# Optimization experiments

Hardware: AMD Instinct MI355X
Metric: run time of the kernel (lower is better)

## Reference

```python
import jax, jax.numpy as jnp
import numpy as np

E, H, NH, FFN, OUT = 4096, 512, 4, 1024, 1
HD = H // NH
LN_EPS = 1e-5


def setup_inputs() -> dict:
    key = jax.random.key(0)
    ks = jax.random.split(key, 20)
    s = 1.0 / np.sqrt(H)
    inp = {
        'x': jax.random.normal(ks[0], (E, H), jnp.float32),
        'edge_index': jax.random.randint(ks[1], (2, E), 0, E, jnp.int64),
        # DMPNN message linear
        'W_msg': jax.random.normal(ks[2], (H, H), jnp.float32) * s,
        'b_msg': jnp.zeros((H,), jnp.float32),
        # GRUCell weights (torch layout: [3H, H], gates r,z,n)
        'W_ih': jax.random.normal(ks[3], (3 * H, H), jnp.float32) * s,
        'b_ih': jnp.zeros((3 * H,), jnp.float32),
        'W_hh': jax.random.normal(ks[4], (3 * H, H), jnp.float32) * s,
        'b_hh': jnp.zeros((3 * H,), jnp.float32),
        # MultiheadAttention combined in-proj [3H, H] and out-proj [H, H]
        'W_in_proj': jax.random.normal(ks[5], (3 * H, H), jnp.float32) * s,
        'b_in_proj': jnp.zeros((3 * H,), jnp.float32),
        'W_out_proj': jax.random.normal(ks[6], (H, H), jnp.float32) * s,
        'b_out_proj': jnp.zeros((H,), jnp.float32),
        # LayerNorm
        'ln_g': jnp.ones((H,), jnp.float32),
        'ln_b': jnp.zeros((H,), jnp.float32),
        # GlobalAttention output linear
        'W_lin': jax.random.normal(ks[7], (H, H), jnp.float32) * s,
        'b_lin': jnp.zeros((H,), jnp.float32),
        # FFN: Linear(H->FFN), ReLU, Linear(FFN->OUT)
        'W_f1': jax.random.normal(ks[8], (FFN, H), jnp.float32) * s,
        'b_f1': jnp.zeros((FFN,), jnp.float32),
        'W_f2': jax.random.normal(ks[9], (OUT, FFN), jnp.float32) * (1.0 / np.sqrt(FFN)),
        'b_f2': jnp.zeros((OUT,), jnp.float32),
    }
    return inp


def reference(x, edge_index, W_msg, b_msg, W_ih, b_ih, W_hh, b_hh,
              W_in_proj, b_in_proj, W_out_proj, b_out_proj, ln_g, ln_b,
              W_lin, b_lin, W_f1, b_f1, W_f2, b_f2):
    # ---- DMPNNLayer: message + scatter-add aggregation + GRUCell update ----
    msg = jax.nn.relu(x @ W_msg.T + b_msg)                       # [E, H]
    agg = jnp.zeros_like(x).at[edge_index[1]].add(msg)           # scatter-add to dst edges
    gi = agg @ W_ih.T + b_ih                                     # [E, 3H]
    gh = x @ W_hh.T + b_hh                                       # [E, 3H]
    ir, iz, inn = jnp.split(gi, 3, axis=-1)
    hr, hz, hn = jnp.split(gh, 3, axis=-1)
    r = jax.nn.sigmoid(ir + hr)
    z = jax.nn.sigmoid(iz + hz)
    n = jnp.tanh(inn + r * hn)
    h = (1.0 - z) * n + z * x                                    # [E, H] updated edges
    # ---- GlobalAttention: MHA(h,h,h) + residual LN + relu(linear) ----
    qkv = h @ W_in_proj.T + b_in_proj                            # [E, 3H]
    q, k, v = jnp.split(qkv, 3, axis=-1)
    split_heads = lambda t: t.reshape(E, NH, HD).transpose(1, 0, 2)  # [NH, E, HD]
    q, k, v = split_heads(q), split_heads(k), split_heads(v)
    scale = np.float32(1.0 / np.sqrt(HD))
    attn = jax.nn.softmax(jnp.einsum('hqd,hkd->hqk', q, k) * scale, axis=-1)
    o = jnp.einsum('hqk,hkd->hqd', attn, v).transpose(1, 0, 2).reshape(E, H)
    o = o @ W_out_proj.T + b_out_proj
    y = o + h
    mu = jnp.mean(y, axis=-1, keepdims=True)
    var = jnp.mean((y - mu) ** 2, axis=-1, keepdims=True)
    yn = (y - mu) / jnp.sqrt(var + LN_EPS) * ln_g + ln_b
    g = jax.nn.relu(yn @ W_lin.T + b_lin)                        # [E, H]
    # ---- FFN ----
    f = jax.nn.relu(g @ W_f1.T + b_f1)                           # [E, FFN]
    return f @ W_f2.T + b_f2                                     # [E, OUT]
```

## Files before the change

### kernel.cpp

```cpp
#include <hip/hip_runtime.h>

typedef unsigned short ushort_t;
typedef __attribute__((ext_vector_type(8))) short short8;
typedef __attribute__((ext_vector_type(4))) float float4v;

#define E_N   4096
#define H_N   512
#define NH_N  4
#define HD_N  128
#define FFN_N 1024
#define H3_N  1536

__device__ __forceinline__ float bf2f(ushort_t u) {
  union { unsigned u; float f; } v; v.u = ((unsigned)u) << 16; return v.f;
}
__device__ __forceinline__ ushort_t f2bf(float f) {
  union { float f; unsigned u; } v; v.f = f;
  unsigned r = v.u + 0x7fffu + ((v.u >> 16) & 1u);
  return (ushort_t)(r >> 16);
}
__device__ __forceinline__ float fexp2(float x) {
  return __builtin_amdgcn_exp2f(x);
}
__device__ __forceinline__ uint4 cvt8(const float* p) {
  float4 a = *(const float4*)p;
  float4 b = *(const float4*)(p + 4);
  union { ushort_t u[8]; uint4 v; } pk;
  pk.u[0] = f2bf(a.x); pk.u[1] = f2bf(a.y); pk.u[2] = f2bf(a.z); pk.u[3] = f2bf(a.w);
  pk.u[4] = f2bf(b.x); pk.u[5] = f2bf(b.y); pk.u[6] = f2bf(b.z); pk.u[7] = f2bf(b.w);
  return pk.v;
}

__device__ __forceinline__ void gload16(const void* g, void* l) {
  __builtin_amdgcn_global_load_lds(
      (const __attribute__((address_space(1))) unsigned*)g,
      (__attribute__((address_space(3))) unsigned*)l, 16, 0, 0);
}

__global__ __launch_bounds__(256) void prep_kernel(
    const float* __restrict__ x,
    const float* __restrict__ wmsg, const float* __restrict__ wih,
    const float* __restrict__ whh,  const float* __restrict__ win,
    const float* __restrict__ wout, const float* __restrict__ wlin,
    const float* __restrict__ wf1,  ushort_t* __restrict__ dst,
    float4* __restrict__ agg)
{
  int b = blockIdx.x;
  if (b < 2048) {
    agg[(size_t)b * 256 + threadIdx.x] = make_float4(0.f, 0.f, 0.f, 0.f);
    return;
  }
  size_t o = ((size_t)(b - 2048) * 256 + threadIdx.x) * 8;
  const float* s;
  if      (o < 2097152) s = x    + o;
  else if (o < 2359296) s = wmsg + (o - 2097152);
  else if (o < 3145728) s = wih  + (o - 2359296);
  else if (o < 3932160) s = whh  + (o - 3145728);
  else if (o < 4718592) s = win  + (o - 3932160);
  else if (o < 4980736) s = wout + (o - 4718592);
  else if (o < 5242880) s = wlin + (o - 4980736);
  else                  s = wf1  + (o - 5242880);
  *(uint4*)(dst + o) = cvt8(s);
}

__global__ __launch_bounds__(256) void cvt_agg_kernel(
    const float* __restrict__ agg, ushort_t* __restrict__ aggb) {
  size_t o = ((size_t)blockIdx.x * 256 + threadIdx.x) * 8;
  *(uint4*)(aggb + o) = cvt8(agg + o);
}

__global__ __launch_bounds__(256) void f2red_kernel(
    const float* __restrict__ pf, const float* __restrict__ b2,
    float* __restrict__ out) {
  int i = blockIdx.x * 256 + threadIdx.x;
  float s = b2[0];
#pragma unroll
  for (int k = 0; k < 32; k++) s += pf[(size_t)i * 32 + k];
  out[i] = s;
}

enum { MODE_MSG = 0, MODE_GI = 1, MODE_GH = 2, MODE_QKV = 3, MODE_OUT = 4,
       MODE_LIN = 5, MODE_F1 = 6 };

template <int MODE, int BM>
__global__ __launch_bounds__(256, (BM == 64 ? 4 : 3)) void gemm_bt(
    const ushort_t* __restrict__ A, const ushort_t* __restrict__ W,
    const float* __restrict__ bias, int K,
    float* __restrict__ outf, ushort_t* __restrict__ outb,
    const int* __restrict__ edge, float* __restrict__ aggf,
    const ushort_t* __restrict__ hres,
    ushort_t* __restrict__ qb, ushort_t* __restrict__ kb,
    ushort_t* __restrict__ vt, const float* __restrict__ wf2)
{
  constexpr int MI   = BM / 32;
  constexpr int ASZ  = BM * 128;
  constexpr int BSZ  = 64 * 128;
  constexpr int NCHA = BM / 8;
  constexpr int NCH  = NCHA + 8;

  __shared__ ushort_t As[2][BM * 64];
  __shared__ ushort_t Bs[2][64 * 64];

  const int tid  = threadIdx.x;
  const int lane = tid & 63;
  const int wave = tid >> 6;
  const int quad = lane >> 4;
  const int l15  = lane & 15;
  const int m0 = blockIdx.x * BM;
  const int n0 = blockIdx.y * 64;
  const int wm = (wave >> 1) * (BM / 2);
  const int wn = (wave & 1) * 32;
  const int rmask = (l15 & 7) << 4;

  const int crow  = lane >> 3;
  const int selem = ((((lane & 7) * 16)) ^ (crow << 4)) >> 1;

  float4v acc[MI][2];
#pragma unroll
  for (int i = 0; i < MI; i++)
#pragma unroll
    for (int j = 0; j < 2; j++)
#pragma unroll
      for (int r = 0; r < 4; r++) acc[i][j][r] = 0.f;

#define ISSUE(KK, BUF)                                                         \
  do {                                                                         \
    _Pragma("unroll")                                                          \
    for (int j_ = 0; j_ < NCH / 4; j_++) {                                     \
      const int c_ = wave + j_ * 4;                                            \
      if (c_ < NCHA) {                                                         \
        const int row_ = c_ * 8 + crow;                                        \
        gload16(A + (size_t)(m0 + row_) * K + (KK) + selem,                    \
                (char*)As + (BUF) * ASZ + c_ * 1024);                          \
      } else {                                                                 \
        const int row_ = (c_ - NCHA) * 8 + crow;                               \
        gload16(W + (size_t)(n0 + row_) * K + (KK) + selem,                    \
                (char*)Bs + (BUF) * BSZ + (c_ - NCHA) * 1024);                 \
      }                                                                        \
    }                                                                          \
  } while (0)

  ISSUE(0, 0);
  int cur = 0;

  for (int k0 = 0; k0 < K; k0 += 64) {
    __syncthreads();
    if (k0 + 64 < K) ISSUE(k0 + 64, cur ^ 1);

#pragma unroll
    for (int ks = 0; ks < 2; ks++) {
      short8 af[MI], bfr[2];
#pragma unroll
      for (int i = 0; i < MI; i++)
        af[i] = *(const short8*)((char*)As + cur * ASZ +
                 (wm + i * 16 + l15) * 128 + ((ks * 64 + quad * 16) ^ rmask));
#pragma unroll
      for (int j = 0; j < 2; j++)
        bfr[j] = *(const short8*)((char*)Bs + cur * BSZ +
                 (wn + j * 16 + l15) * 128 + ((ks * 64 + quad * 16) ^ rmask));
#pragma unroll
      for (int i = 0; i < MI; i++)
#pragma unroll
        for (int j = 0; j < 2; j++)
          acc[i][j] = __builtin_amdgcn_mfma_f32_16x16x32_bf16(af[i], bfr[j],
                                                              acc[i][j], 0, 0, 0);
    }
    cur ^= 1;
  }
#undef ISSUE

  if constexpr (MODE == MODE_F1) {
    float fsum[MI][4];
#pragma unroll
    for (int i = 0; i < MI; i++)
#pragma unroll
      for (int r = 0; r < 4; r++) fsum[i][r] = 0.f;
#pragma unroll
    for (int j = 0; j < 2; j++) {
      const int col = n0 + wn + j * 16 + l15;
      const float bv = bias[col];
      const float wv = wf2[col];
#pragma unroll
      for (int i = 0; i < MI; i++)
#pragma unroll
        for (int r = 0; r < 4; r++)
          fsum[i][r] += fmaxf(acc[i][j][r] + bv, 0.f) * wv;
    }
#pragma unroll
    for (int i = 0; i < MI; i++)
#pragma unroll
      for (int r = 0; r < 4; r++) {
        float s = fsum[i][r];
        s += __shfl_xor(s, 1, 64); s += __shfl_xor(s, 2, 64);
        s += __shfl_xor(s, 4, 64); s += __shfl_xor(s, 8, 64);
        if (l15 == 0)
          outf[(size_t)(m0 + wm + i * 16 + quad * 4 + r) * 32 +
               blockIdx.y * 2 + (wave & 1)] = s;
      }
  } else {
#pragma unroll
    for (int j = 0; j < 2; j++) {
      const int col = n0 + wn + j * 16 + l15;
      const float bv = bias[col];
#pragma unroll
      for (int i = 0; i < MI; i++) {
#pragma unroll
        for (int r = 0; r < 4; r++) {
          const int row = m0 + wm + i * 16 + quad * 4 + r;
          float v = acc[i][j][r] + bv;
          if constexpr (MODE == MODE_MSG) {
            v = fmaxf(v, 0.f);
            const int dst = edge[E_N + row] & (E_N - 1);
            atomicAdd(&aggf[(size_t)dst * H_N + col], v);
          } else if constexpr (MODE == MODE_GI || MODE == MODE_GH) {
            outb[(size_t)row * H3_N + col] = f2bf(v);
          } else if constexpr (MODE == MODE_QKV) {
            const int part = col >> 9;
            const int hh   = (col >> 7) & 3;
            const int d    = col & 127;
            if (part == 0) v *= 0.12751749803605814f;
            const ushort_t bvv = f2bf(v);
            if (part == 0)      qb[((size_t)hh * E_N + row) * HD_N + d] = bvv;
            else if (part == 1) kb[((size_t)hh * E_N + row) * HD_N + d] = bvv;
            else                vt[((size_t)hh * HD_N + d) * E_N + row] = bvv;
          } else if constexpr (MODE == MODE_OUT) {
            v += bf2f(hres[(size_t)row * H_N + col]);
            outf[(size_t)row * H_N + col] = v;
          } else {
            outb[(size_t)row * H_N + col] = f2bf(fmaxf(v, 0.f));
          }
        }
      }
    }
  }
}

__global__ __launch_bounds__(512, 2) void attn_kernel(
    const ushort_t* __restrict__ Qg, const ushort_t* __restrict__ Kg,
    const ushort_t* __restrict__ Vtg, ushort_t* __restrict__ Ob)
{
  const int bid  = blockIdx.x;
  const int head = bid & 3;
  const int qb0  = (bid >> 2) * 64;
  const int tid  = threadIdx.x;
  const int wave = tid >> 6;
  const int grp  = wave >> 2;
  const int w4   = wave & 3;
  const int lane = tid & 63;
  const int quad = lane >> 4;
  const int l15  = lane & 15;

  __shared__ ushort_t Ks[2][2][64][128];
  __shared__ ushort_t Vs[2][2][128][64];
  __shared__ ushort_t Ps[8][16][64];
  char* Psc = (char*)Ps + wave * 2048;

  const ushort_t* Qhead  = Qg  + (size_t)head * E_N * HD_N;
  const ushort_t* Khead  = Kg  + (size_t)head * E_N * HD_N;
  const ushort_t* Vthead = Vtg + (size_t)head * HD_N * E_N;

  short8 aq[4];
#pragma unroll
  for (int ks = 0; ks < 4; ks++)
    aq[ks] = *(const short8*)(Qhead +
        (size_t)(qb0 + w4 * 16 + l15) * HD_N + ks * 32 + quad * 8);

  float4v oacc[8];
#pragma unroll
  for (int i = 0; i < 8; i++)
#pragma unroll
    for (int r = 0; r < 4; r++) oacc[i][r] = 0.f;
  float mprev[4], lsum[4];
#pragma unroll
  for (int r = 0; r < 4; r++) { mprev[r] = -1e30f; lsum[r] = 0.f; }

  const int q15sw = (l15 & 7) << 4;
  const int kt0 = grp * 2048;

#define ISSUE(KT, BUF)                                                         \
  do {                                                                         \
    char* kb_ = (char*)Ks + ((grp * 2 + (BUF)) << 14);                         \
    char* vb_ = (char*)Vs + ((grp * 2 + (BUF)) << 14);                         \
    _Pragma("unroll")                                                          \
    for (int i_ = 0; i_ < 4; i_++) {                                           \
      const int c_ = w4 * 4 + i_;                                              \
      const int krow_ = 4 * c_ + (lane >> 4);              \
      gload16(Khead + (size_t)((KT) + krow_) * HD_N +                          \
                  (((((lane & 15) * 16)) ^ ((krow_ & 7) << 4)) >> 1),          \
              kb_ + c_ * 1024);                                                \
      const int vrow_ = 8 * c_ + (lane >> 3);             \
      gload16(Vthead + (size_t)vrow_ * E_N + (KT) +                            \
                  (((((lane & 7) * 16)) ^ ((lane >> 3) << 4)) >> 1),           \
              vb_ + c_ * 1024);                                                \
    }                                                                          \
  } while (0)

  ISSUE(kt0, 0);
  int cur = 0;

  for (int it = 0; it < 32; it++) {
    __syncthreads();
    if (it + 1 < 32) ISSUE(kt0 + (it + 1) * 64, cur ^ 1);

    const char* kt_ = (char*)Ks + ((grp * 2 + cur) << 14);
    const char* vt_ = (char*)Vs + ((grp * 2 + cur) << 14);

    float4v sacc[4];
#pragma unroll
    for (int j = 0; j < 4; j++)
#pragma unroll
      for (int r = 0; r < 4; r++) sacc[j][r] = 0.f;
#pragma unroll
    for (int ks = 0; ks < 4; ks++) {
#pragma unroll
      for (int j = 0; j < 4; j++) {
        short8 bk = *(const short8*)(kt_ + (j * 16 + l15) * 256 +
                                     ((ks * 64 + quad * 16) ^ q15sw));
        sacc[j] = __builtin_amdgcn_mfma_f32_16x16x32_bf16(aq[ks], bk, sacc[j], 0, 0, 0);
      }
    }

    float alpha[4], pv[4][4];
#pragma unroll
    for (int r = 0; r < 4; r++) {
      float mx = -1e30f;
#pragma unroll
      for (int j = 0; j < 4; j++) { float s = sacc[j][r]; pv[j][r] = s; mx = fmaxf(mx, s); }
#pragma unroll
      for (int off = 1; off < 16; off <<= 1) mx = fmaxf(mx, __shfl_xor(mx, off, 64));
      float mnew = fmaxf(mprev[r], mx);
      alpha[r] = fexp2(mprev[r] - mnew);
      float ss = 0.f;
#pragma unroll
      for (int j = 0; j < 4; j++) { float p = fexp2(pv[j][r] - mnew); pv[j][r] = p; ss += p; }
#pragma unroll
      for (int off = 1; off < 16; off <<= 1) ss += __shfl_xor(ss, off, 64);
      lsum[r] = lsum[r] * alpha[r] + ss;
      mprev[r] = mnew;
    }
#pragma unroll
    for (int i = 0; i < 8; i++)
#pragma unroll
      for (int r = 0; r < 4; r++) oacc[i][r] *= alpha[r];

#pragma unroll
    for (int j = 0; j < 4; j++)
#pragma unroll
      for (int r = 0; r < 4; r++) {
        const int prow = quad * 4 + r;
        *(ushort_t*)(Psc + prow * 128 +
                     ((2 * (j * 16 + l15)) ^ ((prow & 7) << 4))) = f2bf(pv[j][r]);
      }

#pragma unroll
    for (int ks2 = 0; ks2 < 2; ks2++) {
      short8 ap = *(const short8*)(Psc + l15 * 128 +
                                   ((ks2 * 64 + quad * 16) ^ q15sw));
#pragma unroll
      for (int j = 0; j < 8; j++) {
        short8 bv = *(const short8*)(vt_ + (j * 16 + l15) * 128 +
                                     ((ks2 * 64 + quad * 16) ^ q15sw));
        oacc[j] = __builtin_amdgcn_mfma_f32_16x16x32_bf16(ap, bv, oacc[j], 0, 0, 0);
      }
    }
    cur ^= 1;
  }
#undef ISSUE

  __syncthreads();
  float* mO  = (float*)Ks;
  float* mML = (float*)Vs;
  if (grp == 1) {
#pragma unroll
    for (int j = 0; j < 8; j++)
#pragma unroll
      for (int r = 0; r < 4; r++)
        mO[(w4 * 16 + quad * 4 + r) * 128 + j * 16 + l15] = oacc[j][r];
    if (l15 == 0) {
#pragma unroll
      for (int r = 0; r < 4; r++) {
        mML[(w4 * 16 + quad * 4 + r) * 2 + 0] = mprev[r];
        mML[(w4 * 16 + quad * 4 + r) * 2 + 1] = lsum[r];
      }
    }
  }
  __syncthreads();
  if (grp == 0) {
    float s0[4], s1[4];
#pragma unroll
    for (int r = 0; r < 4; r++) {
      int rr = w4 * 16 + quad * 4 + r;
      float m1 = mML[rr * 2 + 0], l1 = mML[rr * 2 + 1];
      float m  = fmaxf(mprev[r], m1);
      float e0 = fexp2(mprev[r] - m);
      float e1 = fexp2(m1 - m);
      float inv = 1.f / (lsum[r] * e0 + l1 * e1);
      s0[r] = e0 * inv;
      s1[r] = e1 * inv;
    }
#pragma unroll
    for (int j = 0; j < 8; j++)
#pragma unroll
      for (int r = 0; r < 4; r++) {
        int row = qb0 + w4 * 16 + quad * 4 + r;
        int col = head * HD_N + j * 16 + l15;
        float o1 = mO[(w4 * 16 + quad * 4 + r) * 128 + j * 16 + l15];
        Ob[(size_t)row * H_N + col] = f2bf(oacc[j][r] * s0[r] + o1 * s1[r]);
      }
  }
}

__global__ __launch_bounds__(256) void gru_kernel(
    const ushort_t* __restrict__ gib, const ushort_t* __restrict__ ghb,
    const float* __restrict__ x, ushort_t* __restrict__ hb) {
  int t = blockIdx.x * 256 + threadIdx.x;
  int e = t >> 6, j8 = (t & 63) * 8;
  size_t b = (size_t)e * H3_N + j8;
  short8 vir = *(const short8*)(gib + b);
  short8 viz = *(const short8*)(gib + b + 512);
  short8 vin = *(const short8*)(gib + b + 1024);
  short8 vhr = *(const short8*)(ghb + b);
  short8 vhz = *(const short8*)(ghb + b + 512);
  short8 vhn = *(const short8*)(ghb + b + 1024);
  size_t xo = (size_t)e * H_N + j8;
  float4 x0 = *(const float4*)(x + xo);
  float4 x1 = *(const float4*)(x + xo + 4);
  float xv[8] = {x0.x, x0.y, x0.z, x0.w, x1.x, x1.y, x1.z, x1.w};
  union { ushort_t u[8]; uint4 v; } o;
#pragma unroll
  for (int i = 0; i < 8; i++) {
    float ir = bf2f((ushort_t)vir[i]), iz = bf2f((ushort_t)viz[i]), inn = bf2f((ushort_t)vin[i]);
    float hr = bf2f((ushort_t)vhr[i]), hz = bf2f((ushort_t)vhz[i]), hn  = bf2f((ushort_t)vhn[i]);
    float r = 1.f / (1.f + __expf(-(ir + hr)));
    float z = 1.f / (1.f + __expf(-(iz + hz)));
    float n = tanhf(inn + r * hn);
    o.u[i] = f2bf((1.f - z) * n + z * xv[i]);
  }
  *(uint4*)(hb + xo) = o.v;
}

__global__ __launch_bounds__(256) void ln_kernel(
    const float* __restrict__ y, const float* __restrict__ g,
    const float* __restrict__ b, ushort_t* __restrict__ yn) {
  int wave = threadIdx.x >> 6, lane = threadIdx.x & 63;
  int row = blockIdx.x * 4 + wave;
  const float* yr = y + (size_t)row * H_N;
  float v[8], s = 0.f;
#pragma unroll
  for (int i = 0; i < 8; i++) { v[i] = yr[lane + i * 64]; s += v[i]; }
#pragma unroll
  for (int off = 1; off < 64; off <<= 1) s += __shfl_xor(s, off, 64);
  float mu = s * (1.f / 512.f);
  float q = 0.f;
#pragma unroll
  for (int i = 0; i < 8; i++) { float d = v[i] - mu; q += d * d; }
#pragma unroll
  for (int off = 1; off < 64; off <<= 1) q += __shfl_xor(q, off, 64);
  float rstd = rsqrtf(q * (1.f / 512.f) + 1e-5f);
#pragma unroll
  for (int i = 0; i < 8; i++) {
    int c = lane + i * 64;
    yn[(size_t)row * H_N + c] = f2bf((v[i] - mu) * rstd * g[c] + b[c]);
  }
}

extern "C" void kernel_launch(void* const* d_in, const int* in_sizes, int n_in,
                              void* d_out, int out_size, void* d_ws, size_t ws_size,
                              hipStream_t stream) {
  const float* x     = (const float*)d_in[0];
  const int*   edge  = (const int*)d_in[1];
  const float* W_msg = (const float*)d_in[2];
  const float* b_msg = (const float*)d_in[3];
  const float* W_ih  = (const float*)d_in[4];
  const float* b_ih  = (const float*)d_in[5];
  const float* W_hh  = (const float*)d_in[6];
  const float* b_hh  = (const float*)d_in[7];
  const float* W_in  = (const float*)d_in[8];
  const float* b_in  = (const float*)d_in[9];
  const float* W_out = (const float*)d_in[10];
  const float* b_out = (const float*)d_in[11];
  const float* ln_g  = (const float*)d_in[12];
  const float* ln_b  = (const float*)d_in[13];
  const float* W_lin = (const float*)d_in[14];
  const float* b_lin = (const float*)d_in[15];
  const float* W_f1  = (const float*)d_in[16];
  const float* b_f1  = (const float*)d_in[17];
  const float* W_f2  = (const float*)d_in[18];
  const float* b_f2  = (const float*)d_in[19];

  char* ws = (char*)d_ws;
  const size_t MB = 1024 * 1024;
  float*    agg  = (float*)(ws + 1 * MB);
  ushort_t* hb   = (ushort_t*)(ws + 1 * MB);
  ushort_t* gib  = (ushort_t*)(ws + 9 * MB);
  ushort_t* ghb  = (ushort_t*)(ws + 21 * MB);
  ushort_t* Qb   = (ushort_t*)(ws + 5 * MB);
  ushort_t* Kb   = (ushort_t*)(ws + 9 * MB);
  ushort_t* Vt   = (ushort_t*)(ws + 13 * MB);
  ushort_t* ob   = (ushort_t*)(ws + 17 * MB);
  float*    y    = (float*)(ws + 21 * MB);
  ushort_t* ynb  = (ushort_t*)(ws + 29 * MB);
  ushort_t* gb   = (ushort_t*)(ws + 31 * MB);
  ushort_t* aggb = (ushort_t*)(ws + 29 * MB);
  float*    pf   = (float*)(ws + 21 * MB);
  ushort_t* xb   = (ushort_t*)(ws + 33 * MB);
  ushort_t* Wmsg_b = xb + 2097152;
  ushort_t* Wih_b  = xb + 2359296;
  ushort_t* Whh_b  = xb + 3145728;
  ushort_t* Win_b  = xb + 3932160;
  ushort_t* Wout_b = xb + 4718592;
  ushort_t* Wlin_b = xb + 4980736;
  ushort_t* Wf1_b  = xb + 5242880;

  prep_kernel<<<4864, 256, 0, stream>>>(
      x, W_msg, W_ih, W_hh, W_in, W_out, W_lin, W_f1, xb, (float4*)agg);

  gemm_bt<MODE_MSG, 64><<<dim3(64, 8), 256, 0, stream>>>(
      xb, Wmsg_b, b_msg, H_N, nullptr, nullptr, edge, agg, nullptr,
      nullptr, nullptr, nullptr, nullptr);

  cvt_agg_kernel<<<1024, 256, 0, stream>>>(agg, aggb);

  gemm_bt<MODE_GI, 128><<<dim3(32, 24), 256, 0, stream>>>(
      aggb, Wih_b, b_ih, H_N, nullptr, gib, nullptr, nullptr, nullptr,
      nullptr, nullptr, nullptr, nullptr);

  gemm_bt<MODE_GH, 128><<<dim3(32, 24), 256, 0, stream>>>(
      xb, Whh_b, b_hh, H_N, nullptr, ghb, nullptr, nullptr, nullptr,
      nullptr, nullptr, nullptr, nullptr);

  gru_kernel<<<1024, 256, 0, stream>>>(gib, ghb, x, hb);

  gemm_bt<MODE_QKV, 128><<<dim3(32, 24), 256, 0, stream>>>(
      hb, Win_b, b_in, H_N, nullptr, nullptr, nullptr, nullptr, nullptr,
      Qb, Kb, Vt, nullptr);

  attn_kernel<<<256, 512, 0, stream>>>(Qb, Kb, Vt, ob);

  gemm_bt<MODE_OUT, 64><<<dim3(64, 8), 256, 0, stream>>>(
      ob, Wout_b, b_out, H_N, y, nullptr, nullptr, nullptr, hb,
      nullptr, nullptr, nullptr, nullptr);

  ln_kernel<<<1024, 256, 0, stream>>>(y, ln_g, ln_b, ynb);

  gemm_bt<MODE_LIN, 64><<<dim3(64, 8), 256, 0, stream>>>(
      ynb, Wlin_b, b_lin, H_N, nullptr, gb, nullptr, nullptr, nullptr,
      nullptr, nullptr, nullptr, nullptr);

  gemm_bt<MODE_F1, 64><<<dim3(64, 16), 256, 0, stream>>>(
      gb, Wf1_b, b_f1, H_N, pf, nullptr, nullptr, nullptr, nullptr,
      nullptr, nullptr, nullptr, W_f2);

  f2red_kernel<<<16, 256, 0, stream>>>(pf, b_f2, (float*)d_out);
}
```

Baseline: 285.6 us.

## Split attention KV halves into separate blocks with global merge kernel

The attention kernel used to run both key halves inside one 512-thread block and merge the partial results through shared memory. Now each half runs as its own 256-thread block, so there are twice as many smaller blocks, each with half the LDS. Each block writes fp32 partial outputs plus max/sum stats to global memory. A new merge kernel then combines them into bf16 output. This aims for better occupancy and scheduling across CUs, at the cost of extra global traffic (about 16 MB of fp32 partials) and one more kernel launch.

```diff
diff --git a/kernel.cpp b/kernel.cpp
--- a/kernel.cpp
+++ b/kernel.cpp
@@ -77,6 +77,33 @@
 #pragma unroll
   for (int k = 0; k < 32; k++) s += pf[(size_t)i * 32 + k];
   out[i] = s;
+}
+
+__global__ __launch_bounds__(256) void amerge_kernel(
+    const float* __restrict__ po0, const float* __restrict__ po1,
+    const float* __restrict__ mlg, ushort_t* __restrict__ ob) {
+  int t = blockIdx.x * 256 + threadIdx.x;
+  int row = t >> 6;
+  int c8  = (t & 63) * 8;
+  int head = c8 >> 7;
+  const float* p0 = mlg + ((size_t)(0 * 4 + head) * E_N + row) * 2;
+  const float* p1 = mlg + ((size_t)(1 * 4 + head) * E_N + row) * 2;
+  float m0 = p0[0], l0 = p0[1], m1 = p1[0], l1 = p1[1];
+  float m  = fmaxf(m0, m1);
+  float e0 = fexp2(m0 - m), e1 = fexp2(m1 - m);
+  float inv = 1.f / (l0 * e0 + l1 * e1);
+  float s0 = e0 * inv, s1 = e1 * inv;
+  size_t off = (size_t)row * H_N + c8;
+  float4 a0 = *(const float4*)(po0 + off);
+  float4 a1 = *(const float4*)(po0 + off + 4);
+  float4 b0 = *(const float4*)(po1 + off);
+  float4 b1 = *(const float4*)(po1 + off + 4);
+  union { ushort_t u[8]; uint4 v; } o;
+  o.u[0] = f2bf(a0.x * s0 + b0.x * s1); o.u[1] = f2bf(a0.y * s0 + b0.y * s1);
+  o.u[2] = f2bf(a0.z * s0 + b0.z * s1); o.u[3] = f2bf(a0.w * s0 + b0.w * s1);
+  o.u[4] = f2bf(a1.x * s0 + b1.x * s1); o.u[5] = f2bf(a1.y * s0 + b1.y * s1);
+  o.u[6] = f2bf(a1.z * s0 + b1.z * s1); o.u[7] = f2bf(a1.w * s0 + b1.w * s1);
+  *(uint4*)(ob + off) = o.v;
 }
 
 enum { MODE_MSG = 0, MODE_GI = 1, MODE_GH = 2, MODE_QKV = 3, MODE_OUT = 4,
@@ -235,24 +262,25 @@
   }
 }
 
-__global__ __launch_bounds__(512, 2) void attn_kernel(
+__global__ __launch_bounds__(256, 2) void attn_kernel(
     const ushort_t* __restrict__ Qg, const ushort_t* __restrict__ Kg,
-    const ushort_t* __restrict__ Vtg, ushort_t* __restrict__ Ob)
+    const ushort_t* __restrict__ Vtg,
+    float* __restrict__ po0, float* __restrict__ po1,
+    float* __restrict__ mlg)
 {
   const int bid  = blockIdx.x;
   const int head = bid & 3;
-  const int qb0  = (bid >> 2) * 64;
+  const int half = (bid >> 2) & 1;
+  const int qb0  = (bid >> 3) * 64;
   const int tid  = threadIdx.x;
   const int wave = tid >> 6;
-  const int grp  = wave >> 2;
-  const int w4   = wave & 3;
   const int lane = tid & 63;
   const int quad = lane >> 4;
   const int l15  = lane & 15;
 
-  __shared__ ushort_t Ks[2][2][64][128];
-  __shared__ ushort_t Vs[2][2][128][64];
-  __shared__ ushort_t Ps[8][16][64];
+  __shared__ ushort_t Ks[2][64][128];
+  __shared__ ushort_t Vs[2][128][64];
+  __shared__ ushort_t Ps[4][16][64];
   char* Psc = (char*)Ps + wave * 2048;
 
   const ushort_t* Qhead  = Qg  + (size_t)head * E_N * HD_N;
@@ -263,7 +291,7 @@
 #pragma unroll
   for (int ks = 0; ks < 4; ks++)
     aq[ks] = *(const short8*)(Qhead +
-        (size_t)(qb0 + w4 * 16 + l15) * HD_N + ks * 32 + quad * 8);
+        (size_t)(qb0 + wave * 16 + l15) * HD_N + ks * 32 + quad * 8);
 
   float4v oacc[8];
 #pragma unroll
@@ -275,15 +303,15 @@
   for (int r = 0; r < 4; r++) { mprev[r] = -1e30f; lsum[r] = 0.f; }
 
   const int q15sw = (l15 & 7) << 4;
-  const int kt0 = grp * 2048;
+  const int kt0 = half * 2048;
 
 #define ISSUE(KT, BUF)                                                         \
   do {                                                                         \
-    char* kb_ = (char*)Ks + ((grp * 2 + (BUF)) << 14);                         \
-    char* vb_ = (char*)Vs + ((grp * 2 + (BUF)) << 14);                         \
+    char* kb_ = (char*)Ks + ((BUF) << 14);                                     \
+    char* vb_ = (char*)Vs + ((BUF) << 14);                                     \
     _Pragma("unroll")                                                          \
     for (int i_ = 0; i_ < 4; i_++) {                                           \
-      const int c_ = w4 * 4 + i_;                                              \
+      const int c_ = wave * 4 + i_;                                            \
       const int krow_ = 4 * c_ + (lane >> 4);              \
       gload16(Khead + (size_t)((KT) + krow_) * HD_N +                          \
                   (((((lane & 15) * 16)) ^ ((krow_ & 7) << 4)) >> 1),          \
@@ -302,8 +330,8 @@
     __syncthreads();
     if (it + 1 < 32) ISSUE(kt0 + (it + 1) * 64, cur ^ 1);
 
-    const char* kt_ = (char*)Ks + ((grp * 2 + cur) << 14);
-    const char* vt_ = (char*)Vs + ((grp * 2 + cur) << 14);
+    const char* kt_ = (char*)Ks + (cur << 14);
+    const char* vt_ = (char*)Vs + (cur << 14);
 
     float4v sacc[4];
 #pragma unroll
@@ -367,46 +395,23 @@
   }
 #undef ISSUE
 
-  __syncthreads();
-  float* mO  = (float*)Ks;
-  float* mML = (float*)Vs;
-  if (grp == 1) {
-#pragma unroll
-    for (int j = 0; j < 8; j++)
-#pragma unroll
-      for (int r = 0; r < 4; r++)
-        mO[(w4 * 16 + quad * 4 + r) * 128 + j * 16 + l15] = oacc[j][r];
-    if (l15 == 0) {
-#pragma unroll
-      for (int r = 0; r < 4; r++) {
-        mML[(w4 * 16 + quad * 4 + r) * 2 + 0] = mprev[r];
-        mML[(w4 * 16 + quad * 4 + r) * 2 + 1] = lsum[r];
-      }
-    }
-  }
-  __syncthreads();
-  if (grp == 0) {
-    float s0[4], s1[4];
+  float* pob = half ? po1 : po0;
+#pragma unroll
+  for (int j = 0; j < 8; j++)
 #pragma unroll
     for (int r = 0; r < 4; r++) {
-      int rr = w4 * 16 + quad * 4 + r;
-      float m1 = mML[rr * 2 + 0], l1 = mML[rr * 2 + 1];
-      float m  = fmaxf(mprev[r], m1);
-      float e0 = fexp2(mprev[r] - m);
-      float e1 = fexp2(m1 - m);
-      float inv = 1.f / (lsum[r] * e0 + l1 * e1);
-      s0[r] = e0 * inv;
-      s1[r] = e1 * inv;
-    }
-#pragma unroll
-    for (int j = 0; j < 8; j++)
-#pragma unroll
-      for (int r = 0; r < 4; r++) {
-        int row = qb0 + w4 * 16 + quad * 4 + r;
-        int col = head * HD_N + j * 16 + l15;
-        float o1 = mO[(w4 * 16 + quad * 4 + r) * 128 + j * 16 + l15];
-        Ob[(size_t)row * H_N + col] = f2bf(oacc[j][r] * s0[r] + o1 * s1[r]);
-      }
+      const int row = qb0 + wave * 16 + quad * 4 + r;
+      const int col = head * HD_N + j * 16 + l15;
+      pob[(size_t)row * H_N + col] = oacc[j][r];
+    }
+  if (l15 == 0) {
+#pragma unroll
+    for (int r = 0; r < 4; r++) {
+      const int row = qb0 + wave * 16 + quad * 4 + r;
+      float* mlp = mlg + ((size_t)(half * 4 + head) * E_N + row) * 2;
+      mlp[0] = mprev[r];
+      mlp[1] = lsum[r];
+    }
   }
 }
 
@@ -503,7 +508,10 @@
   ushort_t* gb   = (ushort_t*)(ws + 31 * MB);
   ushort_t* aggb = (ushort_t*)(ws + 29 * MB);
   float*    pf   = (float*)(ws + 21 * MB);
-  ushort_t* xb   = (ushort_t*)(ws + 33 * MB);
+  float*    po0  = (float*)(ws + 21 * MB);
+  float*    po1  = (float*)(ws + 33 * MB);
+  float*    mlg  = (float*)(ws + 41 * MB);
+  ushort_t* xb   = (ushort_t*)(ws + 42 * MB);
   ushort_t* Wmsg_b = xb + 2097152;
   ushort_t* Wih_b  = xb + 2359296;
   ushort_t* Whh_b  = xb + 3145728;
@@ -535,7 +543,9 @@
       hb, Win_b, b_in, H_N, nullptr, nullptr, nullptr, nullptr, nullptr,
       Qb, Kb, Vt, nullptr);
 
-  attn_kernel<<<256, 512, 0, stream>>>(Qb, Kb, Vt, ob);
+  attn_kernel<<<512, 256, 0, stream>>>(Qb, Kb, Vt, po0, po1, mlg);
+
+  amerge_kernel<<<1024, 256, 0, stream>>>(po0, po1, mlg, ob);
 
   gemm_bt<MODE_OUT, 64><<<dim3(64, 8), 256, 0, stream>>>(
       ob, Wout_b, b_out, H_N, y, nullptr, nullptr, nullptr, hb,
```

After: 284.6 us. Within noise of the previous version (-0.3%).
